# Kernel tuning notes

Measured on AMD Instinct MI355X. Metric: run time of the kernel, lower is better.

The kernel has to match this reference:

```python
import jax, jax.numpy as jnp
import numpy as np

V, E, H, L, B = 32000, 512, 512, 64, 32
H2 = 2 * H  # decoder hidden size
SOS = 127


def lstm_cell(x, h, c, Wih, Whh, b):
    gates = x @ Wih.T + h @ Whh.T + b
    i, f, g, o = jnp.split(gates, 4, axis=-1)
    i = jax.nn.sigmoid(i); f = jax.nn.sigmoid(f); o = jax.nn.sigmoid(o)
    g = jnp.tanh(g)
    c2 = f * c + i * g
    return o * jnp.tanh(c2), c2


def setup_inputs() -> dict:
    key = jax.random.key(0)
    ks = jax.random.split(key, 20)
    s = 0.02
    inp = {
        "x": jax.random.randint(ks[0], (B, L), 0, V),
        "enc_embed": s * jax.random.normal(ks[1], (V, E), jnp.float32),
        "ef_Wih": s * jax.random.normal(ks[2], (4 * H, E), jnp.float32),
        "ef_Whh": s * jax.random.normal(ks[3], (4 * H, H), jnp.float32),
        "ef_b": jnp.zeros((4 * H,), jnp.float32),
        "eb_Wih": s * jax.random.normal(ks[4], (4 * H, E), jnp.float32),
        "eb_Whh": s * jax.random.normal(ks[5], (4 * H, H), jnp.float32),
        "eb_b": jnp.zeros((4 * H,), jnp.float32),
        "dec_embed": s * jax.random.normal(ks[6], (V, H2), jnp.float32),
        "attn_W": s * jax.random.normal(ks[7], (L, 2 * H2), jnp.float32),
        "attn_b": jnp.zeros((L,), jnp.float32),
        "comb_W": s * jax.random.normal(ks[8], (H2, 2 * H2), jnp.float32),
        "comb_b": jnp.zeros((H2,), jnp.float32),
        "d_Wih": s * jax.random.normal(ks[9], (4 * H2, H2), jnp.float32),
        "d_Whh": s * jax.random.normal(ks[10], (4 * H2, H2), jnp.float32),
        "d_b": jnp.zeros((4 * H2,), jnp.float32),
        "out_W": s * jax.random.normal(ks[11], (V, H2), jnp.float32),
        "out_b": jnp.zeros((V,), jnp.float32),
    }
    return inp


def reference(x, enc_embed, ef_Wih, ef_Whh, ef_b, eb_Wih, eb_Whh, eb_b,
              dec_embed, attn_W, attn_b, comb_W, comb_b,
              d_Wih, d_Whh, d_b, out_W, out_b):
    b, seq = x.shape
    emb = enc_embed[x]  # (B, L, E)

    # Encoder: per-timestep bidirectional LSTM cells (each length-1 call),
    # state carried across the unrolled timestep loop.
    def enc_step(carry, xt):
        hf, cf, hb, cb = carry
        hf, cf = lstm_cell(xt, hf, cf, ef_Wih, ef_Whh, ef_b)
        hb, cb = lstm_cell(xt, hb, cb, eb_Wih, eb_Whh, eb_b)
        return (hf, cf, hb, cb), jnp.concatenate([hf, hb], axis=-1)

    z = jnp.zeros((b, ef_Whh.shape[1]), emb.dtype)
    _, enc_outs = jax.lax.scan(enc_step, (z, z, z, z), emb.transpose(1, 0, 2))
    enc_outs = enc_outs.transpose(1, 0, 2)  # (B, L, 2H)

    # Decoder: Bahdanau-style attention + LSTM cell, greedy argmax feedback.
    h2 = d_Whh.shape[1]

    def dec_step(carry, _):
        h, c, tok = carry
        e = dec_embed[tok]  # (B, 2H)
        aw = jax.nn.softmax(jnp.concatenate([e, h], -1) @ attn_W.T + attn_b, axis=-1)  # (B, L)
        ctx = jnp.einsum('bl,bld->bd', aw, enc_outs)  # (B, 2H)
        comb = jax.nn.relu(jnp.concatenate([e, ctx], -1) @ comb_W.T + comb_b)
        h, c = lstm_cell(comb, h, c, d_Wih, d_Whh, d_b)
        logits = jax.nn.log_softmax(h @ out_W.T + out_b, axis=-1)  # (B, V)
        tok = jnp.argmax(logits, axis=-1)
        return (h, c, tok), logits

    h0 = jnp.zeros((b, h2), emb.dtype)
    tok0 = jnp.full((b,), SOS, dtype=x.dtype)
    _, logits = jax.lax.scan(dec_step, (h0, h0, tok0), None, length=seq)
    return logits.transpose(1, 0, 2)  # (B, T, V)
```

## Files before the change

kernel.cpp:

```cpp
#include <hip/hip_runtime.h>
#include <hip/hip_bf16.h>
#include <string.h>

typedef __bf16 bf16;
typedef __attribute__((ext_vector_type(8))) __bf16 bf16x8;
typedef __attribute__((ext_vector_type(2))) __bf16 bf16x2;
typedef __attribute__((ext_vector_type(4))) float  f32x4;
typedef unsigned long long u64;
typedef unsigned char u8;

#define DEV __device__ __forceinline__

constexpr int V = 32000, E = 512, H = 512, L = 64, NB = 32, H2 = 1024, T = 64, SOS = 127;
constexpr int GE = 4 * H;
constexpr int NBLK = 256;

constexpr size_t OFF_GIN    = 0;
constexpr size_t SZ_GIN     = (size_t)2*T*NB*GE*4;
constexpr size_t OFF_ENCOUT = OFF_GIN + SZ_GIN;
constexpr size_t SZ_ENCOUT  = (size_t)NB*L*H2*2;
constexpr size_t OFF_ENCH   = OFF_ENCOUT + SZ_ENCOUT;
constexpr size_t SZ_ENCH    = (size_t)2*2*NB*H*2;
constexpr size_t OFF_DECH   = OFF_ENCH + SZ_ENCH;
constexpr size_t SZ_DECH    = (size_t)2*NB*H2*2;
constexpr size_t OFF_CAT2   = OFF_DECH + SZ_DECH;
constexpr size_t SZ_CAT2    = (size_t)NB*2*H2*2;
constexpr size_t OFF_COMB   = OFF_CAT2 + SZ_CAT2;
constexpr size_t SZ_COMB    = (size_t)NB*H2*2;
constexpr size_t OFF_HH     = OFF_COMB + SZ_COMB;
constexpr size_t SZ_HH      = (size_t)NB*4*H2*4;
constexpr size_t OFF_PMAX   = OFF_HH + SZ_HH;
constexpr size_t SZ_P       = (size_t)4096*NB*4;
constexpr size_t OFF_PSUM   = OFF_PMAX + SZ_P;
constexpr size_t OFF_PIDX   = OFF_PSUM + SZ_P;
constexpr size_t OFF_LOGZ   = OFF_PIDX + SZ_P;
constexpr size_t SZ_LOGZ    = (size_t)T*NB*4;
constexpr size_t OFF_WEFIH  = OFF_LOGZ + SZ_LOGZ;
constexpr size_t SZ_WENC    = (size_t)GE*E*2;
constexpr size_t OFF_WEFHH  = OFF_WEFIH + SZ_WENC;
constexpr size_t OFF_WEBIH  = OFF_WEFHH + SZ_WENC;
constexpr size_t OFF_WEBHH  = OFF_WEBIH + SZ_WENC;
constexpr size_t OFF_WCOMB  = OFF_WEBHH + SZ_WENC;
constexpr size_t SZ_WCOMB   = (size_t)H2*2*H2*2;
constexpr size_t OFF_WDIH   = OFF_WCOMB + SZ_WCOMB;
constexpr size_t SZ_WDEC    = (size_t)4*H2*H2*2;
constexpr size_t OFF_WDHH   = OFF_WDIH + SZ_WDEC;
constexpr size_t OFF_WOUT   = OFF_WDHH + SZ_WDEC;
constexpr size_t OFF_WOUT8  = OFF_WOUT;
constexpr size_t SZ_WOUT8   = (size_t)V*1024;
constexpr size_t OFF_WDHH8  = OFF_WOUT8 + SZ_WOUT8;
constexpr size_t SZ_WOUT    = (size_t)V*H2*2;
constexpr size_t OFF_WATTN  = OFF_WOUT + SZ_WOUT;
constexpr size_t SZ_WATTN   = (size_t)L*2*H2*2;
constexpr size_t OFF_EMB2   = OFF_WATTN + SZ_WATTN;
constexpr size_t SZ_EMB2    = (size_t)T*NB*E*2;
constexpr size_t OFF_BAR    = OFF_EMB2 + SZ_EMB2;
constexpr int BAR_FULLF = 0, BAR_FULLG = 8192, BAR_ENCF = 16384, BAR_ENCG = 18432;
constexpr int BAR_SMF = 20480, BAR_SMG = 22528;
constexpr int BAR_INTS = 24576;
constexpr size_t OFF_H8 = OFF_BAR + 131072;

constexpr int SM_CATF = 65536;
constexpr int SM_REDM = 73728;
constexpr int SM_REDS = 75776;
constexpr int SM_REDI = 77824;
constexpr int SM_SCR  = 79872;
constexpr int SM_HL   = 114688;
constexpr int SM_BYTES = 147456;

DEV f32x4 mfma16(bf16x8 a, bf16x8 b, f32x4 c) {
  return __builtin_amdgcn_mfma_f32_16x16x32_bf16(a, b, c, 0, 0, 0);
}
DEV f32x4 mfma8(long a, long b, f32x4 c) {
  return __builtin_amdgcn_mfma_f32_16x16x32_fp8_fp8(a, b, c, 0, 0, 0);
}
DEV float sigm(float x) { return 1.f / (1.f + __expf(-x)); }
DEV bf16x8 ld8(const bf16* p) { return *(const bf16x8*)p; }

union U16 { u64 u[2]; bf16x8 v8; f32x4 f4; };
union U4  { unsigned int u; bf16x2 v2; float f; };

DEV bf16x8 ld8_dev(const bf16* p) {
  U16 r;
  r.u[0] = __hip_atomic_load((const u64*)p,       __ATOMIC_RELAXED, __HIP_MEMORY_SCOPE_AGENT);
  r.u[1] = __hip_atomic_load((const u64*)(p + 4), __ATOMIC_RELAXED, __HIP_MEMORY_SCOPE_AGENT);
  return r.v8;
}
DEV void st8_dev(bf16* p, bf16x8 v) {
  U16 r; r.v8 = v;
  __hip_atomic_store((u64*)p,       r.u[0], __ATOMIC_RELAXED, __HIP_MEMORY_SCOPE_AGENT);
  __hip_atomic_store((u64*)(p + 4), r.u[1], __ATOMIC_RELAXED, __HIP_MEMORY_SCOPE_AGENT);
}
DEV void st16f_dev(float* p, f32x4 v) {
  U16 r; r.f4 = v;
  __hip_atomic_store((u64*)p,       r.u[0], __ATOMIC_RELAXED, __HIP_MEMORY_SCOPE_AGENT);
  __hip_atomic_store((u64*)(p + 2), r.u[1], __ATOMIC_RELAXED, __HIP_MEMORY_SCOPE_AGENT);
}
DEV float ldf_dev(const float* p) {
  return __hip_atomic_load(p, __ATOMIC_RELAXED, __HIP_MEMORY_SCOPE_AGENT);
}
DEV void stf_dev(float* p, float v) {
  __hip_atomic_store(p, v, __ATOMIC_RELAXED, __HIP_MEMORY_SCOPE_AGENT);
}
DEV int ldi_dev(const int* p) {
  return __hip_atomic_load(p, __ATOMIC_RELAXED, __HIP_MEMORY_SCOPE_AGENT);
}
DEV void sti_dev(int* p, int v) {
  __hip_atomic_store(p, v, __ATOMIC_RELAXED, __HIP_MEMORY_SCOPE_AGENT);
}
DEV void stb_dev(bf16* p, float x) {
  bf16 h = (bf16)x; unsigned short s; memcpy(&s, &h, 2);
  __hip_atomic_store((unsigned short*)p, s, __ATOMIC_RELAXED, __HIP_MEMORY_SCOPE_AGENT);
}
DEV void st2b_dev(bf16* p, bf16x2 v) {
  U4 r; r.v2 = v;
  __hip_atomic_store((unsigned int*)p, r.u, __ATOMIC_RELAXED, __HIP_MEMORY_SCOPE_AGENT);
}
DEV void stb8_dev(u8* p, u8 v) {
  __hip_atomic_store(p, v, __ATOMIC_RELAXED, __HIP_MEMORY_SCOPE_AGENT);
}
DEV u64 ldu64_dev(const u8* p) {
  return __hip_atomic_load((const u64*)p, __ATOMIC_RELAXED, __HIP_MEMORY_SCOPE_AGENT);
}

DEV void fbar(int* flags, int* genA, int nblk, int epoch) {
  __syncthreads();
  if (blockIdx.x == 0) {
    for (int i = threadIdx.x; i < nblk; i += blockDim.x)
      if (i)
        while (__hip_atomic_load(flags + i*32, __ATOMIC_RELAXED, __HIP_MEMORY_SCOPE_AGENT) < epoch)
          __builtin_amdgcn_s_sleep(1);
    __syncthreads();
    for (int i = threadIdx.x; i < nblk; i += blockDim.x)
      __hip_atomic_store(genA + i*32, epoch, __ATOMIC_RELAXED, __HIP_MEMORY_SCOPE_AGENT);
  } else if (threadIdx.x == 0) {
    __hip_atomic_store(flags + blockIdx.x*32, epoch, __ATOMIC_RELAXED, __HIP_MEMORY_SCOPE_AGENT);
    while (__hip_atomic_load(genA + blockIdx.x*32, __ATOMIC_RELAXED, __HIP_MEMORY_SCOPE_AGENT) < epoch)
      __builtin_amdgcn_s_sleep(1);
  }
  asm volatile("" ::: "memory");
  __syncthreads();
}

struct ConvJobs { const float* src[7]; bf16* dst[7]; long n8[7]; };

__global__ __launch_bounds__(256) void k_convert_all(ConvJobs J) {
  long i0 = (long)blockIdx.x * 256 + threadIdx.x;
  long stride = (long)gridDim.x * 256;
  for (int j = 0; j < 7; ++j) {
    const float* __restrict__ src = J.src[j];
    bf16* __restrict__ dst = J.dst[j];
    long n8 = J.n8[j];
    for (long g = i0; g < n8; g += stride) {
      long o = g * 8;
      float4 a = *(const float4*)(src + o);
      float4 b = *(const float4*)(src + o + 4);
      bf16x8 v;
      v[0]=(bf16)a.x; v[1]=(bf16)a.y; v[2]=(bf16)a.z; v[3]=(bf16)a.w;
      v[4]=(bf16)b.x; v[5]=(bf16)b.y; v[6]=(bf16)b.z; v[7]=(bf16)b.w;
      *(bf16x8*)(dst + o) = v;
    }
  }
}

__global__ __launch_bounds__(256) void k_conv_fp8(const float* __restrict__ wsrc,
                                                  const float* __restrict__ hsrc,
                                                  u8* __restrict__ wdst,
                                                  u8* __restrict__ hdst) {
  const long G1 = (long)V*64, G2 = (long)4096*64;
  for (long id = (long)blockIdx.x*256 + threadIdx.x; id < G1 + G2;
       id += (long)gridDim.x*256) {
    const float* s; u8* d; long n, g;
    if (id < G1) { n = id >> 6; g = id & 63; s = wsrc + n*1024 + g*16;
                   d = wdst + n*1024 + ((g ^ (n & 7)) << 4); }
    else { long j = id - G1; n = j >> 6; g = j & 63; s = hsrc + n*1024 + g*16;
           d = hdst + n*1024 + ((g ^ (n & 7)) << 4); }
    unsigned int wv[4];
#pragma unroll
    for (int q = 0; q < 4; ++q) {
      float4 f = *(const float4*)(s + q*4);
      int lo = __builtin_amdgcn_cvt_pk_fp8_f32(f.x*8.f, f.y*8.f, 0, false);
      int hi = __builtin_amdgcn_cvt_pk_fp8_f32(f.z*8.f, f.w*8.f, 0, false);
      wv[q] = (lo & 0xFFFF) | (hi << 16);
    }
    *(uint4*)d = make_uint4(wv[0], wv[1], wv[2], wv[3]);
  }
}

__global__ __launch_bounds__(256) void k_gather_emb(const int* __restrict__ x,
                                                    const float* __restrict__ embed,
                                                    bf16* __restrict__ emb2) {
  int gid = blockIdx.x * 256 + threadIdx.x;
  int m = gid >> 6, k8 = (gid & 63) * 8;
  int b = m & 31, t = m >> 5;
  int tok = x[b * L + t];
  const float* src = embed + (long)tok * E + k8;
  float4 a = *(const float4*)src;
  float4 c = *(const float4*)(src + 4);
  bf16x8 v;
  v[0]=(bf16)a.x; v[1]=(bf16)a.y; v[2]=(bf16)a.z; v[3]=(bf16)a.w;
  v[4]=(bf16)c.x; v[5]=(bf16)c.y; v[6]=(bf16)c.z; v[7]=(bf16)c.w;
  *(bf16x8*)(emb2 + (long)m * E + k8) = v;
}

__global__ __launch_bounds__(256) void k_init(bf16* ench, bf16* dech, float* hh,
                                              int* bar) {
  int i = blockIdx.x * 256 + threadIdx.x;
  hh[i] = 0.f;
  if (i < 2*NB*H)  ench[i] = (bf16)0.f;
  if (i < NB*H2)   dech[i] = (bf16)0.f;
  if (i < BAR_INTS) bar[i] = 0;
}

__global__ __launch_bounds__(256) void k_enc_ingemm(
    const bf16* __restrict__ emb2,
    const bf16* __restrict__ fWih, const float* __restrict__ fB,
    const bf16* __restrict__ bWih, const float* __restrict__ bB,
    float* __restrict__ gin)
{
  int wid  = blockIdx.x * 4 + (threadIdx.x >> 6);
  int lane = threadIdx.x & 63;
  int dir  = wid >> 11;
  int w2   = wid & 2047;
  int m0   = (w2 >> 5) * 32;
  int n0   = (w2 & 31) * 64;
  const bf16*  Wih  = dir ? bWih : fWih;
  const float* Bias = dir ? bB : fB;
  int col = lane & 15, kq = lane >> 4, r4 = kq * 4;

  const bf16* arow[4];
#pragma unroll
  for (int nt = 0; nt < 4; ++nt) arow[nt] = Wih + (long)(n0 + nt*16 + col)*E + kq*8;
  const bf16* brow[2];
#pragma unroll
  for (int mt = 0; mt < 2; ++mt) brow[mt] = emb2 + (long)(m0 + mt*16 + col)*E + kq*8;

  f32x4 acc[2][4] = {};
  for (int kk = 0; kk < E/32; ++kk) {
    bf16x8 a[4], bv[2];
#pragma unroll
    for (int nt = 0; nt < 4; ++nt) a[nt] = ld8(arow[nt] + kk*32);
#pragma unroll
    for (int mt = 0; mt < 2; ++mt) bv[mt] = ld8(brow[mt] + kk*32);
#pragma unroll
    for (int mt = 0; mt < 2; ++mt)
#pragma unroll
      for (int nt = 0; nt < 4; ++nt)
        acc[mt][nt] = mfma16(a[nt], bv[mt], acc[mt][nt]);
  }
#pragma unroll
  for (int mt = 0; mt < 2; ++mt) {
    int m = m0 + mt*16 + col;
    int b = m & 31, t = m >> 5;
    float* gp = gin + ((long)(dir*T + t)*NB + b)*GE;
#pragma unroll
    for (int nt = 0; nt < 4; ++nt) {
      int nb = n0 + nt*16 + r4;
      f32x4 v = acc[mt][nt];
      float4 o;
      o.x = v[0] + Bias[nb+0];
      o.y = v[1] + Bias[nb+1];
      o.z = v[2] + Bias[nb+2];
      o.w = v[3] + Bias[nb+3];
      *(float4*)(gp + nb) = o;
    }
  }
}

struct EncArgs {
  const bf16* fWhh; const bf16* bWhh; const float* gin;
  bf16* ench; bf16* encout; int* flags; int* gen;
};

__global__ __launch_bounds__(256, 1) void k_encoder(EncArgs A) {
  __shared__ float lds[4][16][32];
  int tid = threadIdx.x, w = tid >> 6, lane = tid & 63;
  int dir = blockIdx.x >> 5, j0 = (blockIdx.x & 31) * 16;
  int col = lane & 15, kq = lane >> 4, r4 = kq*4;
  const bf16* Whh = dir ? A.bWhh : A.fWhh;
  const bf16* arow = Whh + (long)(w*H + j0 + col)*H + kq*8;
  float creg0 = 0.f, creg1 = 0.f;

  for (int t = 0; t < T; ++t) {
    const bf16* hbase = A.ench + (t&1)*(2*NB*H) + dir*(NB*H);
    bf16*       hout  = A.ench + ((t&1)^1)*(2*NB*H) + dir*(NB*H);
    const bf16* b0 = hbase + col*H + kq*8;
    const bf16* b1 = hbase + (16+col)*H + kq*8;
    f32x4 a0 = {}, a1 = {};
    for (int kk = 0; kk < H/32; ++kk) {
      bf16x8 a = ld8(arow + kk*32);
      a0 = mfma16(a, ld8_dev(b0 + kk*32), a0);
      a1 = mfma16(a, ld8_dev(b1 + kk*32), a1);
    }
#pragma unroll
    for (int r = 0; r < 4; ++r) { lds[w][r4+r][col] = a0[r]; lds[w][r4+r][16+col] = a1[r]; }
    __syncthreads();
    const float* gp = A.gin + (long)(dir*T + t)*NB*GE;
    {
      int jj = tid >> 5, b = tid & 31, j = j0 + jj;
      const float* g4 = gp + (long)b*GE;
      float i_ = sigm(lds[0][jj][b] + g4[0*H + j]);
      float f_ = sigm(lds[1][jj][b] + g4[1*H + j]);
      float g_ = tanhf(lds[2][jj][b] + g4[2*H + j]);
      float o_ = sigm(lds[3][jj][b] + g4[3*H + j]);
      float c2 = f_*creg0 + i_*g_; creg0 = c2;
      float hv = o_*tanhf(c2);
      stb_dev(hout + b*H + j, hv);
      A.encout[((long)b*L + t)*H2 + dir*H + j] = (bf16)hv;
    }
    {
      int idx = tid + 256, jj = idx >> 5, b = idx & 31, j = j0 + jj;
      const float* g4 = gp + (long)b*GE;
      float i_ = sigm(lds[0][jj][b] + g4[0*H + j]);
      float f_ = sigm(lds[1][jj][b] + g4[1*H + j]);
      float g_ = tanhf(lds[2][jj][b] + g4[2*H + j]);
      float o_ = sigm(lds[3][jj][b] + g4[3*H + j]);
      float c2 = f_*creg1 + i_*g_; creg1 = c2;
      float hv = o_*tanhf(c2);
      stb_dev(hout + b*H + j, hv);
      A.encout[((long)b*L + t)*H2 + dir*H + j] = (bf16)hv;
    }
    fbar(A.flags, A.gen, 64, t + 1);
  }
}

struct DecArgs {
  const float* dec_embed; const bf16* wattn; const float* attn_b;
  const bf16* encout;
  const bf16* wcomb; const float* comb_b;
  const bf16* wdih; const float* db;
  const u8* wout8; const u8* wdhh8; const float* outb;
  bf16* dech; u8* hout8; float* hh; bf16* cat2; bf16* comb;
  float* pmax; float* psum; int* pidx; float* logz; float* out;
  int* fF; int* fG; int* sF; int* sG;
};

__global__ __launch_bounds__(512, 1) void k_decoder(DecArgs A) {
  __shared__ __attribute__((aligned(16))) char smem[SM_BYTES];
  __shared__ float aw[64];
  __shared__ int   stok;
  float* catF = (float*)(smem + SM_CATF);
  float* redm = (float*)(smem + SM_REDM);
  float* reds = (float*)(smem + SM_REDS);
  int*   redi = (int*)  (smem + SM_REDI);
  float* scr  = (float*)(smem + SM_SCR);

  int tid = threadIdx.x, bid = blockIdx.x;
  int w = tid >> 6, lane = tid & 63;
  int col = lane & 15, kq = lane >> 4, r4 = kq*4;
  float creg = 0.f;

  int ntot = (bid < 48) ? 8 : 9;
  int tstart = (bid < 48) ? bid*8 : 384 + 9*(bid - 48);
  int nlds = (bid < 64) ? 4 : 7;

  for (int i = 0; i < nlds; ++i) {
    int tn = tstart + i;
    const u8* src = (tn < 2000) ? A.wout8 + (long)tn*16384
                                : A.wdhh8 + (long)(tn - 2000)*16384;
#pragma unroll
    for (int rr = 0; rr < 2; ++rr) {
      int flat = rr*8192 + w*1024 + lane*16;
      __builtin_amdgcn_global_load_lds(
          (const __attribute__((address_space(1))) void*)(src + flat),
          (__attribute__((address_space(3))) void*)(smem + i*16384 + rr*8192 + w*1024),
          16, 0, 0);
    }
  }
  asm volatile("s_waitcnt vmcnt(0)" ::: "memory");
  __syncthreads();

  for (int t = 0; t < T; ++t) {
    const bf16* hin  = A.dech + (t&1)*(NB*H2);
    bf16*       hout = A.dech + ((t&1)^1)*(NB*H2);

    if (bid < NB) {
      int b = bid;
      if (t > 0) {
        float m = -1e30f, s = 0.f; int id = 0;
        for (int c = tid; c < NBLK; c += 512) {
          float cm = ldf_dev(A.pmax + c*32 + b); int ci = ldi_dev(A.pidx + c*32 + b);
          s += ldf_dev(A.psum + c*32 + b);
          if (cm > m || (cm == m && ci < id)) { m = cm; id = ci; }
        }
        redm[tid] = m; reds[tid] = s; redi[tid] = id;
        __syncthreads();
        for (int off = 256; off; off >>= 1) {
          if (tid < off) {
            float om = redm[tid+off]; int oi = redi[tid+off];
            reds[tid] += reds[tid+off];
            if (om > redm[tid] || (om == redm[tid] && oi < redi[tid])) { redm[tid]=om; redi[tid]=oi; }
          }
          __syncthreads();
        }
        if (tid == 0) { A.logz[(t-1)*32 + b] = logf(reds[0]); stok = redi[0]; }
      } else if (tid == 0) stok = SOS;
      __syncthreads();
      int tok = stok;

      const float* erow = A.dec_embed + (long)tok*H2;
      bf16* c2row = A.cat2 + (long)b*(2*H2);
      if (tid < 128) {
        int o = tid*8;
        float4 a = *(const float4*)(erow + o);
        float4 c = *(const float4*)(erow + o + 4);
        catF[o+0]=a.x; catF[o+1]=a.y; catF[o+2]=a.z; catF[o+3]=a.w;
        catF[o+4]=c.x; catF[o+5]=c.y; catF[o+6]=c.z; catF[o+7]=c.w;
        bf16x8 v;
        v[0]=(bf16)a.x; v[1]=(bf16)a.y; v[2]=(bf16)a.z; v[3]=(bf16)a.w;
        v[4]=(bf16)c.x; v[5]=(bf16)c.y; v[6]=(bf16)c.z; v[7]=(bf16)c.w;
        st8_dev(c2row + o, v);
      } else if (tid < 256) {
        int o = (tid - 128)*8;
        bf16x8 hv = ld8_dev(hin + (long)b*H2 + o);
#pragma unroll
        for (int e = 0; e < 8; ++e) catF[H2 + o + e] = (float)hv[e];
      }
      __syncthreads();

      {
        int l = tid >> 3, q = tid & 7;
        const bf16*  wrow = A.wattn + (long)l*(2*H2) + q*256;
        const float* crow = catF + q*256;
        float sacc = 0.f;
        for (int k = 0; k < 256; k += 8) {
          bf16x8 wv = ld8(wrow + k);
#pragma unroll
          for (int e = 0; e < 8; ++e) sacc += (float)wv[e] * crow[k+e];
        }
        sacc += __shfl_xor(sacc, 1);
        sacc += __shfl_xor(sacc, 2);
        sacc += __shfl_xor(sacc, 4);
        if (q == 0) aw[l] = sacc + A.attn_b[l];
      }
      __syncthreads();

      if (tid < 64) {
        float v = aw[tid];
        float m = v;
#pragma unroll
        for (int off = 1; off < 64; off <<= 1) m = fmaxf(m, __shfl_xor(m, off));
        float p = __expf(v - m);
        float s = p;
#pragma unroll
        for (int off = 1; off < 64; off <<= 1) s += __shfl_xor(s, off);
        aw[tid] = p / s;
      }
      __syncthreads();

      {
        int grp = tid >> 7, jt = tid & 127;
        int j8 = jt * 8;
        const bf16* eo = A.encout + (long)b*L*H2 + j8;
        float acc[8] = {};
        for (int l = grp*16; l < grp*16 + 16; ++l) {
          float a = aw[l];
          bf16x8 v = ld8(eo + (long)l*H2);
#pragma unroll
          for (int e = 0; e < 8; ++e) acc[e] += a*(float)v[e];
        }
#pragma unroll
        for (int e = 0; e < 8; ++e) scr[grp*1024 + j8 + e] = acc[e];
      }
      __syncthreads();
      {
        int j2 = tid * 2;
        bf16x2 o;
#pragma unroll
        for (int e = 0; e < 2; ++e) {
          int j = j2 + e;
          o[e] = (bf16)(scr[j] + scr[1024+j] + scr[2048+j] + scr[3072+j]);
        }
        st2b_dev(c2row + H2 + j2, o);
      }
    }
    if (bid < 64) fbar(A.sF, A.sG, 64, t*2 + 1);

    if (bid < 64) {
      int n0 = bid * 16;
      const bf16* arow = A.wcomb + (long)(n0 + col)*(2*H2) + w*256 + kq*8;
      const bf16* b0 = A.cat2 + (long)col*(2*H2) + w*256 + kq*8;
      const bf16* b1 = A.cat2 + (long)(16+col)*(2*H2) + w*256 + kq*8;
      f32x4 a0 = {}, a1 = {};
      for (int kk = 0; kk < 8; ++kk) {
        bf16x8 a = ld8(arow + kk*32);
        a0 = mfma16(a, ld8_dev(b0 + kk*32), a0);
        a1 = mfma16(a, ld8_dev(b1 + kk*32), a1);
      }
#pragma unroll
      for (int r = 0; r < 4; ++r) {
        scr[(w*2+0)*256 + (r4+r)*16 + col] = a0[r];
        scr[(w*2+1)*256 + (r4+r)*16 + col] = a1[r];
      }
      __syncthreads();
      {
        int r = tid >> 5, b = tid & 31;
        int bt = b >> 4, cb = b & 15;
        float v = 0.f;
#pragma unroll
        for (int g = 0; g < 8; ++g) v += scr[(g*2+bt)*256 + r*16 + cb];
        v += A.comb_b[n0 + r];
        stb_dev(A.comb + (long)b*H2 + n0 + r, fmaxf(v, 0.f));
      }
      fbar(A.sF, A.sG, 64, t*2 + 2);
    }

    if (bid < 64) {
      int j0 = bid * 16;
      int g = w >> 1, half = w & 1;
      const bf16* arow = A.wdih + (long)(g*H2 + j0 + col)*H2 + half*512 + kq*8;
      const bf16* b0 = A.comb + (long)col*H2 + half*512 + kq*8;
      const bf16* b1 = A.comb + (long)(16+col)*H2 + half*512 + kq*8;
      f32x4 a0 = {}, a1 = {};
      for (int kk = 0; kk < 16; ++kk) {
        bf16x8 a = ld8(arow + kk*32);
        a0 = mfma16(a, ld8_dev(b0 + kk*32), a0);
        a1 = mfma16(a, ld8_dev(b1 + kk*32), a1);
      }
#pragma unroll
      for (int r = 0; r < 4; ++r) {
        scr[(w*2+0)*256 + (r4+r)*16 + col] = a0[r];
        scr[(w*2+1)*256 + (r4+r)*16 + col] = a1[r];
      }
      __syncthreads();
      {
        int jj = tid >> 5, b = tid & 31, j = j0 + jj;
        int bt = b >> 4, cb = b & 15;
#define GV(gg) (scr[((2*(gg)+0)*2+bt)*256 + jj*16 + cb] + scr[((2*(gg)+1)*2+bt)*256 + jj*16 + cb] \
                + A.db[(gg)*H2 + j] + ldf_dev(A.hh + (long)b*(4*H2) + (gg)*H2 + j))
        float i_ = sigm(GV(0));
        float f_ = sigm(GV(1));
        float g_ = tanhf(GV(2));
        float o_ = sigm(GV(3));
#undef GV
        float c2 = f_*creg + i_*g_; creg = c2;
        float hv = o_*tanhf(c2);
        stb_dev(hout + b*H2 + j, hv);
        int q8 = __builtin_amdgcn_cvt_pk_fp8_f32(hv*16.f, hv*16.f, 0, false);
        stb8_dev(A.hout8 + b*1024 + j, (u8)(q8 & 0xFF));
      }
    }
    fbar(A.fF, A.fG, 256, t*2 + 1);

    {
#pragma unroll
      for (int k2 = 0; k2 < 4; ++k2) {
        int id = k2*512 + tid;
        int r = id >> 6, g = id & 63;
        const u8* sp = A.hout8 + r*1024 + g*16;
        u64 lo = ldu64_dev(sp);
        u64 hi = ldu64_dev(sp + 8);
        char* dp = smem + SM_HL + r*1024 + ((g ^ (r & 7)) << 4);
        *(u64*)dp = lo; *(u64*)(dp + 8) = hi;
      }
      __syncthreads();

      float pm[2] = {-1e30f, -1e30f};
      float ps[2] = {0.f, 0.f};
      int  pid[2] = {0, 0};

      for (int ii = 0; ii < 2; ++ii) {
        if (ii == 1 && (w != 0 || ntot < 9)) break;
        int ti = (ii == 0) ? w : 8;
        int tn = tstart + ti;
        f32x4 acc0 = {}, acc1 = {};
        if (ti < nlds) {
          const char* Ab = smem + ti*16384 + col*1024;
          const char* Hb = smem + SM_HL + col*1024;
#pragma unroll 8
          for (int ks = 0; ks < 32; ++ks) {
            int off = (((ks*2 + (kq>>1)) ^ (col & 7)) << 4) + (kq & 1)*8;
            long a  = *(const long*)(Ab + off);
            long b0 = *(const long*)(Hb + off);
            long b1 = *(const long*)(Hb + 16*1024 + off);
            acc0 = mfma8(a, b0, acc0);
            acc1 = mfma8(a, b1, acc1);
          }
        } else {
          const u8* Ab = ((tn < 2000) ? A.wout8 + (long)tn*16384
                                      : A.wdhh8 + (long)(tn - 2000)*16384) + col*1024;
          const char* Hb = smem + SM_HL + col*1024;
#pragma unroll 8
          for (int ks = 0; ks < 32; ++ks) {
            int off = (((ks*2 + (kq>>1)) ^ (col & 7)) << 4) + (kq & 1)*8;
            long a  = *(const long*)(Ab + off);
            long b0 = *(const long*)(Hb + off);
            long b1 = *(const long*)(Hb + 16*1024 + off);
            acc0 = mfma8(a, b0, acc0);
            acc1 = mfma8(a, b1, acc1);
          }
        }
        if (tn < 2000) {
          int nb = tn*16 + kq*4;
#pragma unroll
          for (int bt = 0; bt < 2; ++bt) {
            int b = col + bt*16;
            f32x4 v = bt ? acc1 : acc0;
            f32x4 o;
#pragma unroll
            for (int r = 0; r < 4; ++r) {
              float xv = v[r]*0.0078125f + A.outb[nb + r];
              o[r] = xv;
              ps[bt] += __expf(xv);
              if (xv > pm[bt]) { pm[bt] = xv; pid[bt] = nb + r; }
            }
            __builtin_nontemporal_store(o, (f32x4*)(A.out + ((long)b*T + t)*V + nb));
          }
        } else {
          int nb = (tn - 2000)*16 + kq*4;
#pragma unroll
          for (int bt = 0; bt < 2; ++bt) {
            int b = col + bt*16;
            f32x4 v = bt ? acc1 : acc0;
#pragma unroll
            for (int r = 0; r < 4; ++r) v[r] *= 0.0078125f;
            st16f_dev(A.hh + (long)b*(4*H2) + nb, v);
          }
        }
      }
#pragma unroll
      for (int off = 16; off <= 32; off <<= 1) {
#pragma unroll
        for (int bt = 0; bt < 2; ++bt) {
          float om = __shfl_xor(pm[bt], off);
          float os = __shfl_xor(ps[bt], off);
          int   oi = __shfl_xor(pid[bt], off);
          ps[bt] += os;
          if (om > pm[bt] || (om == pm[bt] && oi < pid[bt])) { pm[bt] = om; pid[bt] = oi; }
        }
      }
      __syncthreads();
      float* dm = (float*)(smem + SM_HL);
      float* ds = dm + 256;
      int*   di = (int*)(ds + 256);
      if (lane < 16) {
#pragma unroll
        for (int bt = 0; bt < 2; ++bt) {
          int b = bt*16 + lane;
          dm[w*32 + b] = pm[bt];
          ds[w*32 + b] = ps[bt];
          di[w*32 + b] = pid[bt];
        }
      }
      __syncthreads();
      if (tid < 32) {
        int b = tid;
        float m = -1e30f, s = 0.f; int id = 0;
#pragma unroll
        for (int r = 0; r < 8; ++r) {
          float om = dm[r*32 + b]; int oi = di[r*32 + b];
          s += ds[r*32 + b];
          if (om > m || (om == m && oi < id)) { m = om; id = oi; }
        }
        stf_dev(A.pmax + bid*32 + b, m);
        stf_dev(A.psum + bid*32 + b, s);
        sti_dev(A.pidx + bid*32 + b, id);
      }
    }
    fbar(A.fF, A.fG, 256, t*2 + 2);
  }

  if (bid < NB) {
    int b = bid;
    float s = 0.f;
    for (int c = tid; c < NBLK; c += 512) s += ldf_dev(A.psum + c*32 + b);
    reds[tid] = s;
    __syncthreads();
    for (int off = 256; off; off >>= 1) {
      if (tid < off) reds[tid] += reds[tid+off];
      __syncthreads();
    }
    if (tid == 0) A.logz[(T-1)*32 + b] = logf(reds[0]);
  }
}

__global__ __launch_bounds__(256) void k_fixup(float* __restrict__ out,
                                               const float* __restrict__ logz)
{
  long i = (long)blockIdx.x * 256 + threadIdx.x;
  long stride = (long)gridDim.x * 256;
  long total = (long)NB * T * V / 4;
  for (long g = i; g < total; g += stride) {
    long flat = g * 4;
    long bt = flat / V;
    int tt = (int)(bt & 63), b = (int)(bt >> 6);
    float lz = logz[tt*32 + b];
    f32x4 v = *(const f32x4*)(out + flat);
    v[0] -= lz; v[1] -= lz; v[2] -= lz; v[3] -= lz;
    __builtin_nontemporal_store(v, (f32x4*)(out + flat));
  }
}

extern "C" void kernel_launch(void* const* d_in, const int* in_sizes, int n_in,
                              void* d_out, int out_size, void* d_ws, size_t ws_size,
                              hipStream_t stream)
{
  const int*   x         = (const int*)  d_in[0];
  const float* enc_embed = (const float*)d_in[1];
  const float* ef_Wih    = (const float*)d_in[2];
  const float* ef_Whh    = (const float*)d_in[3];
  const float* ef_b      = (const float*)d_in[4];
  const float* eb_Wih    = (const float*)d_in[5];
  const float* eb_Whh    = (const float*)d_in[6];
  const float* eb_b      = (const float*)d_in[7];
  const float* dec_embed = (const float*)d_in[8];
  const float* attn_W    = (const float*)d_in[9];
  const float* attn_b    = (const float*)d_in[10];
  const float* comb_W    = (const float*)d_in[11];
  const float* comb_b    = (const float*)d_in[12];
  const float* d_Wih     = (const float*)d_in[13];
  const float* d_Whh     = (const float*)d_in[14];
  const float* d_b       = (const float*)d_in[15];
  const float* out_W     = (const float*)d_in[16];
  const float* out_b     = (const float*)d_in[17];
  float* out = (float*)d_out;
  char* ws = (char*)d_ws;

  float* gin    = (float*)(ws + OFF_GIN);
  bf16*  encout = (bf16*) (ws + OFF_ENCOUT);
  bf16*  ench   = (bf16*) (ws + OFF_ENCH);
  bf16*  dech   = (bf16*) (ws + OFF_DECH);
  bf16*  cat2   = (bf16*) (ws + OFF_CAT2);
  bf16*  comb   = (bf16*) (ws + OFF_COMB);
  float* hh     = (float*)(ws + OFF_HH);
  float* pmax   = (float*)(ws + OFF_PMAX);
  float* psum   = (float*)(ws + OFF_PSUM);
  int*   pidx   = (int*)  (ws + OFF_PIDX);
  float* logz   = (float*)(ws + OFF_LOGZ);
  bf16*  wefih  = (bf16*) (ws + OFF_WEFIH);
  bf16*  wefhh  = (bf16*) (ws + OFF_WEFHH);
  bf16*  webih  = (bf16*) (ws + OFF_WEBIH);
  bf16*  webhh  = (bf16*) (ws + OFF_WEBHH);
  bf16*  wcomb  = (bf16*) (ws + OFF_WCOMB);
  bf16*  wdih   = (bf16*) (ws + OFF_WDIH);
  u8*    wout8  = (u8*)   (ws + OFF_WOUT8);
  u8*    wdhh8  = (u8*)   (ws + OFF_WDHH8);
  bf16*  wattn  = (bf16*) (ws + OFF_WATTN);
  bf16*  emb2   = (bf16*) (ws + OFF_EMB2);
  int*   bar    = (int*)  (ws + OFF_BAR);
  u8*    hout8  = (u8*)   (ws + OFF_H8);

  ConvJobs J;
  J.src[0]=ef_Wih; J.dst[0]=wefih; J.n8[0]=(long)GE*E/8;
  J.src[1]=ef_Whh; J.dst[1]=wefhh; J.n8[1]=(long)GE*H/8;
  J.src[2]=eb_Wih; J.dst[2]=webih; J.n8[2]=(long)GE*E/8;
  J.src[3]=eb_Whh; J.dst[3]=webhh; J.n8[3]=(long)GE*H/8;
  J.src[4]=comb_W; J.dst[4]=wcomb; J.n8[4]=(long)H2*2*H2/8;
  J.src[5]=d_Wih;  J.dst[5]=wdih;  J.n8[5]=(long)4*H2*H2/8;
  J.src[6]=attn_W; J.dst[6]=wattn; J.n8[6]=(long)L*2*H2/8;
  hipLaunchKernelGGL(k_convert_all, dim3(2048), dim3(256), 0, stream, J);
  hipLaunchKernelGGL(k_conv_fp8, dim3(2048), dim3(256), 0, stream,
                     out_W, d_Whh, wout8, wdhh8);
  hipLaunchKernelGGL(k_gather_emb, dim3(512), dim3(256), 0, stream, x, enc_embed, emb2);
  hipLaunchKernelGGL(k_init, dim3(512), dim3(256), 0, stream, ench, dech, hh, bar);
  hipLaunchKernelGGL(k_enc_ingemm, dim3(1024), dim3(256), 0, stream,
                     emb2, wefih, ef_b, webih, eb_b, gin);

  EncArgs EA = { wefhh, webhh, gin, ench, encout,
                 bar + BAR_ENCF, bar + BAR_ENCG };
  hipLaunchKernelGGL(k_encoder, dim3(64), dim3(256), 0, stream, EA);

  DecArgs DA = { dec_embed, wattn, attn_b, encout, wcomb, comb_b,
                 wdih, d_b, wout8, wdhh8, out_b,
                 dech, hout8, hh, cat2, comb, pmax, psum, pidx, logz, out,
                 bar + BAR_FULLF, bar + BAR_FULLG, bar + BAR_SMF, bar + BAR_SMG };
  hipLaunchKernelGGL(k_decoder, dim3(256), dim3(512), 0, stream, DA);

  hipLaunchKernelGGL(k_fixup, dim3(2048), dim3(256), 0, stream, out, logz);
}
```

Measured before the change: 5.277 ms.

## Replace centralized grid barriers with per-stage producer tag publish/wait

Replaces the two-level grid barrier (block 0 gathers flags, then releases everyone) with per-block epoch tags. Each stage publishes its own tag and consumers wait only on the producer blocks they need. The partial max/sum/idx buffers are double-buffered by timestep parity so the next step's writers do not race with readers. This removes barrier round trips and lets blocks outside the dependency set run ahead. The cost is more fine-grained polling and a higher risk of subtle ordering bugs, since only relaxed atomics and a compiler fence are used.

Result: no change. 5.212 ms (-1.2%).

```diff
diff --git a/kernel.cpp b/kernel.cpp
--- a/kernel.cpp
+++ b/kernel.cpp
@@ -30,7 +30,7 @@
 constexpr size_t OFF_HH     = OFF_COMB + SZ_COMB;
 constexpr size_t SZ_HH      = (size_t)NB*4*H2*4;
 constexpr size_t OFF_PMAX   = OFF_HH + SZ_HH;
-constexpr size_t SZ_P       = (size_t)4096*NB*4;
+constexpr size_t SZ_P       = (size_t)2*NBLK*NB*4;
 constexpr size_t OFF_PSUM   = OFF_PMAX + SZ_P;
 constexpr size_t OFF_PIDX   = OFF_PSUM + SZ_P;
 constexpr size_t OFF_LOGZ   = OFF_PIDX + SZ_P;
@@ -55,9 +55,8 @@
 constexpr size_t OFF_EMB2   = OFF_WATTN + SZ_WATTN;
 constexpr size_t SZ_EMB2    = (size_t)T*NB*E*2;
 constexpr size_t OFF_BAR    = OFF_EMB2 + SZ_EMB2;
-constexpr int BAR_FULLF = 0, BAR_FULLG = 8192, BAR_ENCF = 16384, BAR_ENCG = 18432;
-constexpr int BAR_SMF = 20480, BAR_SMG = 22528;
-constexpr int BAR_INTS = 24576;
+constexpr int TAG_PT = 0, TAG_C2 = 8192, TAG_CB = 9216, TAG_H = 11264, TAG_E = 13312;
+constexpr int BAR_INTS = 15360;
 constexpr size_t OFF_H8 = OFF_BAR + 131072;
 
 constexpr int SM_CATF = 65536;
@@ -123,21 +122,15 @@
   return __hip_atomic_load((const u64*)p, __ATOMIC_RELAXED, __HIP_MEMORY_SCOPE_AGENT);
 }
 
-DEV void fbar(int* flags, int* genA, int nblk, int epoch) {
+DEV void tpub(int* tags, int slot, int ep) {
   __syncthreads();
-  if (blockIdx.x == 0) {
-    for (int i = threadIdx.x; i < nblk; i += blockDim.x)
-      if (i)
-        while (__hip_atomic_load(flags + i*32, __ATOMIC_RELAXED, __HIP_MEMORY_SCOPE_AGENT) < epoch)
-          __builtin_amdgcn_s_sleep(1);
-    __syncthreads();
-    for (int i = threadIdx.x; i < nblk; i += blockDim.x)
-      __hip_atomic_store(genA + i*32, epoch, __ATOMIC_RELAXED, __HIP_MEMORY_SCOPE_AGENT);
-  } else if (threadIdx.x == 0) {
-    __hip_atomic_store(flags + blockIdx.x*32, epoch, __ATOMIC_RELAXED, __HIP_MEMORY_SCOPE_AGENT);
-    while (__hip_atomic_load(genA + blockIdx.x*32, __ATOMIC_RELAXED, __HIP_MEMORY_SCOPE_AGENT) < epoch)
+  if (threadIdx.x == 0)
+    sti_dev(tags + slot*32, ep);
+}
+DEV void twait(int* tags, int n, int ep) {
+  if ((int)threadIdx.x < n)
+    while (ldi_dev(tags + threadIdx.x*32) < ep)
       __builtin_amdgcn_s_sleep(1);
-  }
   asm volatile("" ::: "memory");
   __syncthreads();
 }
@@ -269,7 +262,7 @@
 
 struct EncArgs {
   const bf16* fWhh; const bf16* bWhh; const float* gin;
-  bf16* ench; bf16* encout; int* flags; int* gen;
+  bf16* ench; bf16* encout; int* etag;
 };
 
 __global__ __launch_bounds__(256, 1) void k_encoder(EncArgs A) {
@@ -279,9 +272,11 @@
   int col = lane & 15, kq = lane >> 4, r4 = kq*4;
   const bf16* Whh = dir ? A.bWhh : A.fWhh;
   const bf16* arow = Whh + (long)(w*H + j0 + col)*H + kq*8;
+  int* myTags = A.etag + dir*32*32;
   float creg0 = 0.f, creg1 = 0.f;
 
   for (int t = 0; t < T; ++t) {
+    if (t > 0) twait(myTags, 32, t);
     const bf16* hbase = A.ench + (t&1)*(2*NB*H) + dir*(NB*H);
     bf16*       hout  = A.ench + ((t&1)^1)*(2*NB*H) + dir*(NB*H);
     const bf16* b0 = hbase + col*H + kq*8;
@@ -320,7 +315,7 @@
       stb_dev(hout + b*H + j, hv);
       A.encout[((long)b*L + t)*H2 + dir*H + j] = (bf16)hv;
     }
-    fbar(A.flags, A.gen, 64, t + 1);
+    tpub(myTags, blockIdx.x & 31, t + 1);
   }
 }
 
@@ -332,7 +327,7 @@
   const u8* wout8; const u8* wdhh8; const float* outb;
   bf16* dech; u8* hout8; float* hh; bf16* cat2; bf16* comb;
   float* pmax; float* psum; int* pidx; float* logz; float* out;
-  int* fF; int* fG; int* sF; int* sG;
+  int* tags;
 };
 
 __global__ __launch_bounds__(512, 1) void k_decoder(DecArgs A) {
@@ -345,6 +340,11 @@
   int*   redi = (int*)  (smem + SM_REDI);
   float* scr  = (float*)(smem + SM_SCR);
 
+  int* PT  = A.tags + TAG_PT;
+  int* C2T = A.tags + TAG_C2;
+  int* CBT = A.tags + TAG_CB;
+  int* HT  = A.tags + TAG_H;
+
   int tid = threadIdx.x, bid = blockIdx.x;
   int w = tid >> 6, lane = tid & 63;
   int col = lane & 15, kq = lane >> 4, r4 = kq*4;
@@ -373,14 +373,18 @@
   for (int t = 0; t < T; ++t) {
     const bf16* hin  = A.dech + (t&1)*(NB*H2);
     bf16*       hout = A.dech + ((t&1)^1)*(NB*H2);
+    float* pmaxP = A.pmax + ((t&1)^1)*NBLK*32;
+    float* psumP = A.psum + ((t&1)^1)*NBLK*32;
+    int*   pidxP = A.pidx + ((t&1)^1)*NBLK*32;
 
     if (bid < NB) {
       int b = bid;
       if (t > 0) {
+        twait(PT, NBLK, t);
         float m = -1e30f, s = 0.f; int id = 0;
         for (int c = tid; c < NBLK; c += 512) {
-          float cm = ldf_dev(A.pmax + c*32 + b); int ci = ldi_dev(A.pidx + c*32 + b);
-          s += ldf_dev(A.psum + c*32 + b);
+          float cm = ldf_dev(pmaxP + c*32 + b); int ci = ldi_dev(pidxP + c*32 + b);
+          s += ldf_dev(psumP + c*32 + b);
           if (cm > m || (cm == m && ci < id)) { m = cm; id = ci; }
         }
         redm[tid] = m; reds[tid] = s; redi[tid] = id;
@@ -473,10 +477,11 @@
         }
         st2b_dev(c2row + H2 + j2, o);
       }
-    }
-    if (bid < 64) fbar(A.sF, A.sG, 64, t*2 + 1);
+      tpub(C2T, bid, t + 1);
+    }
 
     if (bid < 64) {
+      twait(C2T, 32, t + 1);
       int n0 = bid * 16;
       const bf16* arow = A.wcomb + (long)(n0 + col)*(2*H2) + w*256 + kq*8;
       const bf16* b0 = A.cat2 + (long)col*(2*H2) + w*256 + kq*8;
@@ -502,10 +507,11 @@
         v += A.comb_b[n0 + r];
         stb_dev(A.comb + (long)b*H2 + n0 + r, fmaxf(v, 0.f));
       }
-      fbar(A.sF, A.sG, 64, t*2 + 2);
+      tpub(CBT, bid, t + 1);
     }
 
     if (bid < 64) {
+      twait(CBT, 64, t + 1);
       int j0 = bid * 16;
       int g = w >> 1, half = w & 1;
       const bf16* arow = A.wdih + (long)(g*H2 + j0 + col)*H2 + half*512 + kq*8;
@@ -539,10 +545,15 @@
         int q8 = __builtin_amdgcn_cvt_pk_fp8_f32(hv*16.f, hv*16.f, 0, false);
         stb8_dev(A.hout8 + b*1024 + j, (u8)(q8 & 0xFF));
       }
-    }
-    fbar(A.fF, A.fG, 256, t*2 + 1);
+      tpub(HT, bid, t + 1);
+    }
 
     {
+      twait(HT, 64, t + 1);
+      float* pmaxW = A.pmax + (t&1)*NBLK*32;
+      float* psumW = A.psum + (t&1)*NBLK*32;
+      int*   pidxW = A.pidx + (t&1)*NBLK*32;
+
 #pragma unroll
       for (int k2 = 0; k2 < 4; ++k2) {
         int id = k2*512 + tid;
@@ -652,18 +663,20 @@
           s += ds[r*32 + b];
           if (om > m || (om == m && oi < id)) { m = om; id = oi; }
         }
-        stf_dev(A.pmax + bid*32 + b, m);
-        stf_dev(A.psum + bid*32 + b, s);
-        sti_dev(A.pidx + bid*32 + b, id);
-      }
-    }
-    fbar(A.fF, A.fG, 256, t*2 + 2);
+        stf_dev(pmaxW + bid*32 + b, m);
+        stf_dev(psumW + bid*32 + b, s);
+        sti_dev(pidxW + bid*32 + b, id);
+      }
+      tpub(PT, bid, t + 1);
+    }
   }
 
   if (bid < NB) {
+    twait(PT, NBLK, T);
     int b = bid;
+    const float* psumP = A.psum + ((T-1)&1)*NBLK*32;
     float s = 0.f;
-    for (int c = tid; c < NBLK; c += 512) s += ldf_dev(A.psum + c*32 + b);
+    for (int c = tid; c < NBLK; c += 512) s += ldf_dev(psumP + c*32 + b);
     reds[tid] = s;
     __syncthreads();
     for (int off = 256; off; off >>= 1) {
@@ -756,14 +769,13 @@
   hipLaunchKernelGGL(k_enc_ingemm, dim3(1024), dim3(256), 0, stream,
                      emb2, wefih, ef_b, webih, eb_b, gin);
 
-  EncArgs EA = { wefhh, webhh, gin, ench, encout,
-                 bar + BAR_ENCF, bar + BAR_ENCG };
+  EncArgs EA = { wefhh, webhh, gin, ench, encout, bar + TAG_E };
   hipLaunchKernelGGL(k_encoder, dim3(64), dim3(256), 0, stream, EA);
 
   DecArgs DA = { dec_embed, wattn, attn_b, encout, wcomb, comb_b,
                  wdih, d_b, wout8, wdhh8, out_b,
                  dech, hout8, hh, cat2, comb, pmax, psum, pidx, logz, out,
-                 bar + BAR_FULLF, bar + BAR_FULLG, bar + BAR_SMF, bar + BAR_SMG };
+                 bar };
   hipLaunchKernelGGL(k_decoder, dim3(256), dim3(512), 0, stream, DA);
 
   hipLaunchKernelGGL(k_fixup, dim3(2048), dim3(256), 0, stream, out, logz);
```
